# Kernel optimization log

Measured on AMD Instinct MI355X. Metric: run time of the kernel, lower is better.

Reference implementation:

```python
import jax, jax.numpy as jnp
import numpy as np

DIM = 768
NUM_EXPERTS = 1536
EXPERT_DIM = 64
NOISE_SCALE = 0.1
B, H, W = 1, 64, 64
N = B * H * W


def setup_inputs() -> dict:
    key = jax.random.key(0)
    ks = jax.random.split(key, 6)
    scaled = lambda k, shape, fan_in: (jax.random.normal(k, shape, jnp.float32) / np.sqrt(fan_in)).astype(jnp.float32)
    return {
        "x": jax.random.normal(ks[0], (B, H, W, DIM), jnp.float32),
        "noise": jax.random.normal(ks[1], (N, NUM_EXPERTS), jnp.float32),
        "gate_w": scaled(ks[2], (NUM_EXPERTS, DIM), DIM),
        "gate_b": jnp.zeros((NUM_EXPERTS,), jnp.float32),
        "expert_w": scaled(ks[3], (NUM_EXPERTS, EXPERT_DIM, DIM), DIM),  # torch Linear weight layout (out, in)
        "expert_b": jnp.zeros((NUM_EXPERTS, EXPERT_DIM), jnp.float32),
        "proj_w": scaled(ks[4], (DIM, EXPERT_DIM), EXPERT_DIM),
        "proj_b": jnp.zeros((DIM,), jnp.float32),
    }


def reference(x, noise, gate_w, gate_b, expert_w, expert_b, proj_w, proj_b):
    orig_shape = x.shape
    xf = x.reshape(-1, orig_shape[-1])  # (N, DIM)
    # Noisy gating
    scores = xf @ gate_w.T + gate_b + noise * NOISE_SCALE  # (N, E)
    gate_weights = jax.nn.softmax(scores, axis=-1)
    top_w, top_i = jax.lax.top_k(gate_weights, 1)  # (N, 1), (N, 1)
    idx = top_i[:, 0]  # (N,)
    # Gather only the selected expert per token (same math as the redundant
    # dense all-expert compute followed by a gather in the original).
    w_sel = expert_w[idx]  # (N, EXPERT_DIM, DIM)
    b_sel = expert_b[idx]  # (N, EXPERT_DIM)
    y = jnp.einsum('nd,nod->no', xf, w_sel) + b_sel  # (N, EXPERT_DIM)
    out_flat = (y @ proj_w.T + proj_b) * top_w  # (N, DIM); top_w broadcasts (N,1)
    return out_flat.reshape(orig_shape)
```

## Files before the change

### kernel.cpp

```cpp
#include <hip/hip_runtime.h>
#include <hip/hip_bf16.h>

#define NT 4096
#define DIM 768
#define NE 1536
#define ED 64
#define GAP_THR 8e-3f

typedef __attribute__((ext_vector_type(8))) short short8v;
typedef __attribute__((ext_vector_type(4))) float f32x4;

__device__ __forceinline__ unsigned short f2bf(float f) {
  unsigned int u = __float_as_uint(f);
  unsigned int r = (u + 0x7fffu + ((u >> 16) & 1u)) >> 16;
  return (unsigned short)r;
}
__device__ __forceinline__ float bf2f(unsigned short h) {
  return __uint_as_float(((unsigned int)h) << 16);
}

__device__ __forceinline__ void gload16(const void* g, void* l) {
  __builtin_amdgcn_global_load_lds((const __attribute__((address_space(1))) void*)g,
                                   (__attribute__((address_space(3))) void*)l, 16, 0, 0);
}

__device__ __forceinline__ void top2_merge(float& m1, int& i1, float& m2, int& i2,
                                           float om1, int oi1, float om2, int oi2) {
  if (om1 > m1 || (om1 == m1 && oi1 < i1)) {
    if (m1 > om2 || (m1 == om2 && i1 < oi2)) { m2 = m1; i2 = i1; }
    else { m2 = om2; i2 = oi2; }
    m1 = om1; i1 = oi1;
  } else {
    if (om1 > m2 || (om1 == m2 && oi1 < i2)) { m2 = om1; i2 = oi1; }
  }
}

__global__ __launch_bounds__(256) void split_all(
    const float* __restrict__ x, const float* __restrict__ gw,
    unsigned short* __restrict__ xhi, unsigned short* __restrict__ xlo,
    unsigned short* __restrict__ ghi, unsigned short* __restrict__ glo,
    int* __restrict__ rc_cnt) {
  if (blockIdx.x == 0 && threadIdx.x == 0) *rc_cnt = 0;
  const int nx4 = NT * DIM / 4;
  const int ng4 = NE * DIM / 4;
  int i = blockIdx.x * 256 + threadIdx.x;
  const float* src; unsigned short* hi; unsigned short* lo; int j;
  if (i < nx4) { src = x; hi = xhi; lo = xlo; j = i; }
  else { j = i - nx4; if (j >= ng4) return; src = gw; hi = ghi; lo = glo; }
  float4 v = ((const float4*)src)[j];
  unsigned short h0 = f2bf(v.x), h1 = f2bf(v.y), h2 = f2bf(v.z), h3 = f2bf(v.w);
  ((ushort4*)hi)[j] = make_ushort4(h0, h1, h2, h3);
  ((ushort4*)lo)[j] = make_ushort4(f2bf(v.x - bf2f(h0)), f2bf(v.y - bf2f(h1)),
                                   f2bf(v.z - bf2f(h2)), f2bf(v.w - bf2f(h3)));
}

__global__ __launch_bounds__(256) void gate_mfma(
    const unsigned short* __restrict__ xhi, const unsigned short* __restrict__ xlo,
    const unsigned short* __restrict__ ghi, const unsigned short* __restrict__ glo,
    const float* __restrict__ gb, const float* __restrict__ noise,
    float4* __restrict__ part_a, int* __restrict__ part_i2) {
  __shared__ __align__(16) unsigned short sA[2 * 128 * 32];
  __shared__ __align__(16) unsigned short sB[2 * 128 * 32];
  const int tid = threadIdx.x;
  const int w = tid >> 6, lane = tid & 63;
  const int wr = w >> 1, wc = w & 1;
  const int bm = blockIdx.x, bn = blockIdx.y;
  const int fr = lane & 15;
  const int fg = lane >> 4;
  const int gsw = fg ^ ((fr >> 1) & 3);

  f32x4 acc[4][4];
#pragma unroll
  for (int i = 0; i < 4; i++)
#pragma unroll
    for (int j = 0; j < 4; j++) acc[i][j] = (f32x4){0.f, 0.f, 0.f, 0.f};

  const size_t arow = (size_t)bm * 128 * DIM;
  const size_t brow = (size_t)bn * 128 * DIM;
  const int sr_lo = tid >> 2;
  const int sg = (tid & 3) ^ ((tid >> 3) & 3);

  for (int kt = 0; kt < DIM; kt += 32) {
    __syncthreads();
#pragma unroll
    for (int h = 0; h < 2; h++) {
      const int r = h * 64 + sr_lo;
      const size_t asrc = arow + (size_t)r * DIM + kt + sg * 8;
      const size_t bsrc = brow + (size_t)r * DIM + kt + sg * 8;
      const int dofs = h * 2048 + w * 512;
      gload16(xhi + asrc, &sA[dofs]);
      gload16(xlo + asrc, &sA[4096 + dofs]);
      gload16(ghi + bsrc, &sB[dofs]);
      gload16(glo + bsrc, &sB[4096 + dofs]);
    }
    __syncthreads();

    short8v ah[4], al[4], bh[4], bl[4];
#pragma unroll
    for (int mf = 0; mf < 4; mf++) {
      int ro = (wr * 64 + mf * 16 + fr) * 32 + gsw * 8;
      ah[mf] = *(const short8v*)&sA[ro];
      al[mf] = *(const short8v*)&sA[4096 + ro];
    }
#pragma unroll
    for (int nf = 0; nf < 4; nf++) {
      int ro = (wc * 64 + nf * 16 + fr) * 32 + gsw * 8;
      bh[nf] = *(const short8v*)&sB[ro];
      bl[nf] = *(const short8v*)&sB[4096 + ro];
    }
#pragma unroll
    for (int mf = 0; mf < 4; mf++)
#pragma unroll
      for (int nf = 0; nf < 4; nf++) {
        f32x4 c = acc[mf][nf];
        c = __builtin_amdgcn_mfma_f32_16x16x32_bf16(ah[mf], bh[nf], c, 0, 0, 0);
        c = __builtin_amdgcn_mfma_f32_16x16x32_bf16(ah[mf], bl[nf], c, 0, 0, 0);
        c = __builtin_amdgcn_mfma_f32_16x16x32_bf16(al[mf], bh[nf], c, 0, 0, 0);
        acc[mf][nf] = c;
      }
  }

  const int gm0 = bm * 128 + wr * 64;
  const int gn0 = bn * 128 + wc * 64;
  const int chunk = bn * 2 + wc;
  int gcol[4]; float gbv[4];
#pragma unroll
  for (int nf = 0; nf < 4; nf++) { gcol[nf] = gn0 + nf * 16 + fr; gbv[nf] = gb[gcol[nf]]; }
#pragma unroll
  for (int mf = 0; mf < 4; mf++) {
    float sv[4][4];
#pragma unroll
    for (int nf = 0; nf < 4; nf++)
#pragma unroll
      for (int reg = 0; reg < 4; reg++) {
        int gm = gm0 + mf * 16 + fg * 4 + reg;
        sv[nf][reg] = acc[mf][nf][reg] + gbv[nf] + 0.1f * noise[(size_t)gm * NE + gcol[nf]];
      }
#pragma unroll
    for (int reg = 0; reg < 4; reg++) {
      float m1 = sv[0][reg]; int i1 = gcol[0];
      float m2 = -3e38f; int i2 = 0x7fffffff;
#pragma unroll
      for (int nf = 1; nf < 4; nf++) {
        float v = sv[nf][reg]; int ii = gcol[nf];
        if (v > m1 || (v == m1 && ii < i1)) { m2 = m1; i2 = i1; m1 = v; i1 = ii; }
        else if (v > m2 || (v == m2 && ii < i2)) { m2 = v; i2 = ii; }
      }
#pragma unroll
      for (int off = 1; off <= 8; off <<= 1) {
        float om1 = __shfl_xor(m1, off, 64); int oi1 = __shfl_xor(i1, off, 64);
        float om2 = __shfl_xor(m2, off, 64); int oi2 = __shfl_xor(i2, off, 64);
        top2_merge(m1, i1, m2, i2, om1, oi1, om2, oi2);
      }
      float ssum = 0.f;
#pragma unroll
      for (int nf = 0; nf < 4; nf++) ssum += __expf(sv[nf][reg] - m1);
#pragma unroll
      for (int off = 1; off <= 8; off <<= 1) ssum += __shfl_xor(ssum, off, 64);
      if (fr == 0) {
        int gm = gm0 + mf * 16 + fg * 4 + reg;
        part_a[(size_t)gm * 24 + chunk] = make_float4(m1, m2, ssum, __int_as_float(i1));
        part_i2[(size_t)gm * 24 + chunk] = i2;
      }
    }
  }
}

__global__ __launch_bounds__(256) void finalize(
    const float4* __restrict__ part_a, const int* __restrict__ part_i2,
    float* __restrict__ topw, int* __restrict__ idx,
    int* __restrict__ rc_count, int* __restrict__ rc_n, int* __restrict__ rc_i2) {
  const int wv = threadIdx.x >> 6, lane = threadIdx.x & 63;
  const int n = blockIdx.x * 4 + wv;
  float m1 = -3e38f, m2 = -3e38f, lm1 = -3e38f, lsum = 0.f;
  int i1 = 0x7fffffff, i2 = 0x7fffffff;
  if (lane < 24) {
    float4 pa = part_a[(size_t)n * 24 + lane];
    m1 = pa.x; m2 = pa.y; lsum = pa.z; i1 = __float_as_int(pa.w);
    i2 = part_i2[(size_t)n * 24 + lane];
    lm1 = pa.x;
  }
#pragma unroll
  for (int off = 1; off <= 32; off <<= 1) {
    float om1 = __shfl_xor(m1, off, 64); int oi1 = __shfl_xor(i1, off, 64);
    float om2 = __shfl_xor(m2, off, 64); int oi2 = __shfl_xor(i2, off, 64);
    top2_merge(m1, i1, m2, i2, om1, oi1, om2, oi2);
  }
  float contrib = (lane < 24) ? __expf(lm1 - m1) * lsum : 0.f;
#pragma unroll
  for (int off = 1; off <= 32; off <<= 1) contrib += __shfl_xor(contrib, off, 64);
  if (lane == 0) {
    topw[n] = 1.0f / contrib;
    idx[n] = i1;
    if (m1 - m2 < GAP_THR) {
      int p = atomicAdd(rc_count, 1);
      rc_n[p] = n; rc_i2[p] = i2;
    }
  }
}

__global__ __launch_bounds__(256) void recheck(
    const float* __restrict__ x, const float* __restrict__ gw,
    const float* __restrict__ gb, const float* __restrict__ noise,
    const int* __restrict__ rc_n, const int* __restrict__ rc_i2,
    const int* __restrict__ rc_count, int* __restrict__ idx) {
  __shared__ float r1[4], r2[4];
  const int cnt = *rc_count;
  const int tid = threadIdx.x;
  const int w = tid >> 6, lane = tid & 63;
  for (int t = blockIdx.x; t < cnt; t += gridDim.x) {
    const int n = rc_n[t];
    const int e1 = idx[n], e2 = rc_i2[t];
    const float* xr = x + (size_t)n * DIM;
    const float* w1 = gw + (size_t)e1 * DIM;
    const float* w2 = gw + (size_t)e2 * DIM;
    float p1 = 0.f, p2 = 0.f;
    for (int k = tid; k < DIM; k += 256) {
      float xv = xr[k];
      p1 += xv * w1[k];
      p2 += xv * w2[k];
    }
#pragma unroll
    for (int off = 32; off; off >>= 1) {
      p1 += __shfl_xor(p1, off, 64);
      p2 += __shfl_xor(p2, off, 64);
    }
    if (lane == 0) { r1[w] = p1; r2[w] = p2; }
    __syncthreads();
    if (tid == 0) {
      float s1 = r1[0] + r1[1] + r1[2] + r1[3] + gb[e1] + 0.1f * noise[(size_t)n * NE + e1];
      float s2 = r2[0] + r2[1] + r2[2] + r2[3] + gb[e2] + 0.1f * noise[(size_t)n * NE + e2];
      if (s2 > s1 || (s2 == s1 && e2 < e1)) idx[n] = e2;
    }
    __syncthreads();
  }
}

__global__ __launch_bounds__(256) void expert_y(
    const float* __restrict__ x, const float* __restrict__ ew,
    const float* __restrict__ eb, const int* __restrict__ idx,
    float* __restrict__ y) {
  const int e = blockIdx.x;
  __shared__ int toklist[128];
  __shared__ int ntok_s;
  __shared__ __align__(16) float xs[8][DIM];
  const int tid = threadIdx.x;
  const int w = tid >> 6, lane = tid & 63;

  if (tid == 0) ntok_s = 0;
  __syncthreads();
  for (int q = tid; q < NT / 4; q += 256) {
    int4 v = ((const int4*)idx)[q];
    int n0 = q * 4;
    if (v.x == e) toklist[atomicAdd(&ntok_s, 1) & 127] = n0;
    if (v.y == e) toklist[atomicAdd(&ntok_s, 1) & 127] = n0 + 1;
    if (v.z == e) toklist[atomicAdd(&ntok_s, 1) & 127] = n0 + 2;
    if (v.w == e) toklist[atomicAdd(&ntok_s, 1) & 127] = n0 + 3;
  }
  __syncthreads();
  const int cnt = min(ntok_s, 128);
  if (cnt == 0) return;

  const float4* W4 = (const float4*)(ew + (size_t)e * ED * DIM);
  const float4* X4 = (const float4*)x;
  const float4* Wc = W4 + w * 3072;

  for (int c0 = 0; c0 < cnt; c0 += 8) {
    const int cc = min(8, cnt - c0);
    __syncthreads();
    for (int f = tid; f < cc * 192; f += 256) {
      int t = f / 192, p = f - t * 192;
      *(float4*)&xs[t][p * 4] = X4[(size_t)toklist[c0 + t] * 192 + p];
    }
    __syncthreads();

    int tok_l[8];
#pragma unroll
    for (int t = 0; t < 8; t++) tok_l[t] = toklist[(c0 + t) & 127];

    f32x4 xf[3][8];
#pragma unroll
    for (int b = 0; b < 3; b++)
#pragma unroll
      for (int t = 0; t < 8; t++)
        xf[b][t] = (t < cc) ? *(const f32x4*)&xs[t][(b * 64 + lane) * 4]
                            : (f32x4){0.f, 0.f, 0.f, 0.f};

    for (int a = 0; a < 16; a++) {
      f32x4 wv0 = *(const f32x4*)&Wc[a * 192 + lane];
      f32x4 wv1 = *(const f32x4*)&Wc[a * 192 + 64 + lane];
      f32x4 wv2 = *(const f32x4*)&Wc[a * 192 + 128 + lane];
      float p[8];
#pragma unroll
      for (int t = 0; t < 8; t++) {
        p[t] = wv0.x * xf[0][t].x + wv0.y * xf[0][t].y + wv0.z * xf[0][t].z + wv0.w * xf[0][t].w
             + wv1.x * xf[1][t].x + wv1.y * xf[1][t].y + wv1.z * xf[1][t].z + wv1.w * xf[1][t].w
             + wv2.x * xf[2][t].x + wv2.y * xf[2][t].y + wv2.z * xf[2][t].z + wv2.w * xf[2][t].w;
      }
      const int o = w * 16 + a;
      const float ebv = eb[e * ED + o];
#pragma unroll
      for (int t = 0; t < 8; t++) {
        if (t < cc) {
          float r = p[t];
          r += __shfl_xor(r, 1, 64);
          r += __shfl_xor(r, 2, 64);
          r += __shfl_xor(r, 4, 64);
          r += __shfl_xor(r, 8, 64);
          r += __shfl_xor(r, 16, 64);
          r += __shfl_xor(r, 32, 64);
          if (lane == 0) y[(size_t)tok_l[t] * ED + o] = r + ebv;
        }
      }
    }
  }
}

__global__ __launch_bounds__(256) void proj_kernel(
    const float* __restrict__ y, const float* __restrict__ pw,
    const float* __restrict__ pb, const float* __restrict__ topw,
    float* __restrict__ out) {
  const int b = blockIdx.x;
  const int tid = threadIdx.x;
  __shared__ float4 ys4[8 * 16];
  __shared__ float tw[8];
  if (tid < 128) {
    int t = tid >> 4, q = tid & 15;
    ys4[tid] = ((const float4*)y)[((size_t)b * 8 + t) * 16 + q];
  }
  if (tid < 8) tw[tid] = topw[b * 8 + tid];
  __syncthreads();
  const float4* pw4 = (const float4*)pw;
#pragma unroll
  for (int c = 0; c < 3; c++) {
    int d = c * 256 + tid;
    float4 pwv[16];
#pragma unroll
    for (int q = 0; q < 16; q++) pwv[q] = pw4[(size_t)d * 16 + q];
    float pbv = pb[d];
    for (int t = 0; t < 8; t++) {
      const float4* yv4 = &ys4[t * 16];
      float s = 0.f;
#pragma unroll
      for (int q = 0; q < 16; q++) {
        float4 yv = yv4[q];
        s += pwv[q].x * yv.x + pwv[q].y * yv.y + pwv[q].z * yv.z + pwv[q].w * yv.w;
      }
      out[((size_t)b * 8 + t) * DIM + d] = (s + pbv) * tw[t];
    }
  }
}

extern "C" void kernel_launch(void* const* d_in, const int* in_sizes, int n_in,
                              void* d_out, int out_size, void* d_ws, size_t ws_size,
                              hipStream_t stream) {
  const float* x      = (const float*)d_in[0];
  const float* noise  = (const float*)d_in[1];
  const float* gate_w = (const float*)d_in[2];
  const float* gate_b = (const float*)d_in[3];
  const float* ew     = (const float*)d_in[4];
  const float* eb     = (const float*)d_in[5];
  const float* pw     = (const float*)d_in[6];
  const float* pb     = (const float*)d_in[7];
  float* out = (float*)d_out;

  char* ws = (char*)d_ws;
  unsigned short* xhi    = (unsigned short*)(ws);
  unsigned short* xlo    = (unsigned short*)(ws + 6291456);
  unsigned short* ghi    = (unsigned short*)(ws + 12582912);
  unsigned short* glo    = (unsigned short*)(ws + 14942208);
  float4*         part_a = (float4*)(ws + 17301504);
  int*            part_i2= (int*)  (ws + 18874368);
  float*          y      = (float*)(ws + 19267584);
  float*          topw   = (float*)(ws + 20316160);
  int*            idx    = (int*)  (ws + 20332544);
  int*            rc_cnt = (int*)  (ws + 20348928);
  int*            rc_n   = (int*)  (ws + 20349184);
  int*            rc_i2  = (int*)  (ws + 20365568);

  split_all<<<(NT * DIM / 4 + NE * DIM / 4 + 255) / 256, 256, 0, stream>>>(
      x, gate_w, xhi, xlo, ghi, glo, rc_cnt);
  gate_mfma<<<dim3(NT / 128, NE / 128), 256, 0, stream>>>(
      xhi, xlo, ghi, glo, gate_b, noise, part_a, part_i2);
  finalize<<<NT / 4, 256, 0, stream>>>(part_a, part_i2, topw, idx,
                                       rc_cnt, rc_n, rc_i2);
  recheck<<<64, 256, 0, stream>>>(x, gate_w, gate_b, noise, rc_n, rc_i2, rc_cnt, idx);
  expert_y<<<NE, 256, 0, stream>>>(x, ew, eb, idx, y);
  proj_kernel<<<NT / 8, 256, 0, stream>>>(y, pw, pb, topw, out);
}
```

Measured before the change: 251.8 us.

## Split expert matvec over input-dim slices with partial sums reduced in proj

The expert kernel grid becomes a 2D grid that splits each expert's 768-wide dot products into three 256-wide slices, each writing a separate partial y buffer. x is read straight from global memory instead of being staged in LDS. The projection kernel sums the three partial buffers when it loads y. This adds parallelism and removes LDS staging and barriers, but it triples the per-block idx scan and adds partial-buffer traffic.

```diff
diff --git a/kernel.cpp b/kernel.cpp
--- a/kernel.cpp
+++ b/kernel.cpp
@@ -239,11 +239,10 @@
 __global__ __launch_bounds__(256) void expert_y(
     const float* __restrict__ x, const float* __restrict__ ew,
     const float* __restrict__ eb, const int* __restrict__ idx,
-    float* __restrict__ y) {
-  const int e = blockIdx.x;
+    float* __restrict__ yp) {
+  const int e = blockIdx.x, s = blockIdx.y;
   __shared__ int toklist[128];
   __shared__ int ntok_s;
-  __shared__ __align__(16) float xs[8][DIM];
   const int tid = threadIdx.x;
   const int w = tid >> 6, lane = tid & 63;
 
@@ -263,42 +262,28 @@
 
   const float4* W4 = (const float4*)(ew + (size_t)e * ED * DIM);
   const float4* X4 = (const float4*)x;
-  const float4* Wc = W4 + w * 3072;
+  float* ypo = yp + (size_t)s * NT * ED;
 
   for (int c0 = 0; c0 < cnt; c0 += 8) {
     const int cc = min(8, cnt - c0);
-    __syncthreads();
-    for (int f = tid; f < cc * 192; f += 256) {
-      int t = f / 192, p = f - t * 192;
-      *(float4*)&xs[t][p * 4] = X4[(size_t)toklist[c0 + t] * 192 + p];
-    }
-    __syncthreads();
-
     int tok_l[8];
 #pragma unroll
     for (int t = 0; t < 8; t++) tok_l[t] = toklist[(c0 + t) & 127];
 
-    f32x4 xf[3][8];
-#pragma unroll
-    for (int b = 0; b < 3; b++)
+    f32x4 xf[8];
+#pragma unroll
+    for (int t = 0; t < 8; t++)
+      xf[t] = (t < cc) ? *(const f32x4*)&X4[(size_t)tok_l[t] * 192 + s * 64 + lane]
+                       : (f32x4){0.f, 0.f, 0.f, 0.f};
+
+    for (int a = 0; a < 16; a++) {
+      const int o = w * 16 + a;
+      f32x4 wv = *(const f32x4*)&W4[(size_t)o * 192 + s * 64 + lane];
+      float p[8];
 #pragma unroll
       for (int t = 0; t < 8; t++)
-        xf[b][t] = (t < cc) ? *(const f32x4*)&xs[t][(b * 64 + lane) * 4]
-                            : (f32x4){0.f, 0.f, 0.f, 0.f};
-
-    for (int a = 0; a < 16; a++) {
-      f32x4 wv0 = *(const f32x4*)&Wc[a * 192 + lane];
-      f32x4 wv1 = *(const f32x4*)&Wc[a * 192 + 64 + lane];
-      f32x4 wv2 = *(const f32x4*)&Wc[a * 192 + 128 + lane];
-      float p[8];
-#pragma unroll
-      for (int t = 0; t < 8; t++) {
-        p[t] = wv0.x * xf[0][t].x + wv0.y * xf[0][t].y + wv0.z * xf[0][t].z + wv0.w * xf[0][t].w
-             + wv1.x * xf[1][t].x + wv1.y * xf[1][t].y + wv1.z * xf[1][t].z + wv1.w * xf[1][t].w
-             + wv2.x * xf[2][t].x + wv2.y * xf[2][t].y + wv2.z * xf[2][t].z + wv2.w * xf[2][t].w;
-      }
-      const int o = w * 16 + a;
-      const float ebv = eb[e * ED + o];
+        p[t] = wv.x * xf[t].x + wv.y * xf[t].y + wv.z * xf[t].z + wv.w * xf[t].w;
+      const float ebv = (s == 0) ? eb[e * ED + o] : 0.f;
 #pragma unroll
       for (int t = 0; t < 8; t++) {
         if (t < cc) {
@@ -309,7 +294,7 @@
           r += __shfl_xor(r, 8, 64);
           r += __shfl_xor(r, 16, 64);
           r += __shfl_xor(r, 32, 64);
-          if (lane == 0) y[(size_t)tok_l[t] * ED + o] = r + ebv;
+          if (lane == 0) ypo[(size_t)tok_l[t] * ED + o] = r + ebv;
         }
       }
     }
@@ -317,16 +302,22 @@
 }
 
 __global__ __launch_bounds__(256) void proj_kernel(
-    const float* __restrict__ y, const float* __restrict__ pw,
+    const float* __restrict__ yp, const float* __restrict__ pw,
     const float* __restrict__ pb, const float* __restrict__ topw,
     float* __restrict__ out) {
   const int b = blockIdx.x;
   const int tid = threadIdx.x;
   __shared__ float4 ys4[8 * 16];
   __shared__ float tw[8];
+  const float4* yp0 = (const float4*)yp;
+  const float4* yp1 = (const float4*)(yp + (size_t)NT * ED);
+  const float4* yp2 = (const float4*)(yp + (size_t)2 * NT * ED);
   if (tid < 128) {
     int t = tid >> 4, q = tid & 15;
-    ys4[tid] = ((const float4*)y)[((size_t)b * 8 + t) * 16 + q];
+    size_t i = ((size_t)b * 8 + t) * 16 + q;
+    float4 a = yp0[i], c = yp1[i], d = yp2[i];
+    ys4[tid] = make_float4(a.x + c.x + d.x, a.y + c.y + d.y,
+                           a.z + c.z + d.z, a.w + c.w + d.w);
   }
   if (tid < 8) tw[tid] = topw[b * 8 + tid];
   __syncthreads();
@@ -371,12 +362,12 @@
   unsigned short* glo    = (unsigned short*)(ws + 14942208);
   float4*         part_a = (float4*)(ws + 17301504);
   int*            part_i2= (int*)  (ws + 18874368);
-  float*          y      = (float*)(ws + 19267584);
-  float*          topw   = (float*)(ws + 20316160);
-  int*            idx    = (int*)  (ws + 20332544);
-  int*            rc_cnt = (int*)  (ws + 20348928);
-  int*            rc_n   = (int*)  (ws + 20349184);
-  int*            rc_i2  = (int*)  (ws + 20365568);
+  float*          yp     = (float*)(ws + 19267584);
+  float*          topw   = (float*)(ws + 22413312);
+  int*            idx    = (int*)  (ws + 22429696);
+  int*            rc_cnt = (int*)  (ws + 22446080);
+  int*            rc_n   = (int*)  (ws + 22446336);
+  int*            rc_i2  = (int*)  (ws + 22462720);
 
   split_all<<<(NT * DIM / 4 + NE * DIM / 4 + 255) / 256, 256, 0, stream>>>(
       x, gate_w, xhi, xlo, ghi, glo, rc_cnt);
@@ -385,6 +376,6 @@
   finalize<<<NT / 4, 256, 0, stream>>>(part_a, part_i2, topw, idx,
                                        rc_cnt, rc_n, rc_i2);
   recheck<<<64, 256, 0, stream>>>(x, gate_w, gate_b, noise, rc_n, rc_i2, rc_cnt, idx);
-  expert_y<<<NE, 256, 0, stream>>>(x, ew, eb, idx, y);
-  proj_kernel<<<NT / 8, 256, 0, stream>>>(y, pw, pb, topw, out);
-}
+  expert_y<<<dim3(NE, 3), 256, 0, stream>>>(x, ew, eb, idx, yp);
+  proj_kernel<<<NT / 8, 256, 0, stream>>>(yp, pw, pb, topw, out);
+}
```

Result: slower. 295.9 us (+17.5%).
